# Kernel tuning notes

Measured on AMD Instinct MI355X. Metric: run time of the kernel, lower is better.

The kernel has to match this reference:

```python
import jax, jax.numpy as jnp
import numpy as np

EPS = 1e-5  # BatchNorm eps (torch default)

def setup_inputs() -> dict:
    key = jax.random.key(0)
    ks = jax.random.split(key, 12)
    B, C, H, W = 4, 256, 64, 64
    IC = 128  # inter_channels = C // 2
    s = 1.0 / np.sqrt(C)
    si = 1.0 / np.sqrt(IC)
    return {
        "x": jax.random.normal(ks[0], (B, C, H, W), jnp.float32),
        "y": jax.random.normal(ks[1], (B, C, H, W), jnp.float32),
        "g_w": jax.random.normal(ks[2], (IC, C), jnp.float32) * s,
        "g_b": jax.random.normal(ks[3], (IC,), jnp.float32) * 0.01,
        "dx_w": jax.random.normal(ks[4], (IC, C), jnp.float32) * s,
        "dx_b": jax.random.normal(ks[5], (IC,), jnp.float32) * 0.01,
        "dy_w": jax.random.normal(ks[6], (IC, C), jnp.float32) * s,
        "dy_b": jax.random.normal(ks[7], (IC,), jnp.float32) * 0.01,
        "w_w": jax.random.normal(ks[8], (C, IC), jnp.float32) * si,
        "w_b": jax.random.normal(ks[9], (C,), jnp.float32) * 0.01,
        "bn_gamma": jax.random.normal(ks[10], (C,), jnp.float32),
        "bn_beta": jax.random.normal(ks[11], (C,), jnp.float32) * 0.01,
    }

def _conv1x1(t, w, b):
    # t: [B,C,H,W], w: [O,C], b: [O] -> [B,O,H,W]
    return jnp.einsum('bchw,oc->bohw', t, w) + b[None, :, None, None]

def reference(x, y, g_w, g_b, dx_w, dx_b, dy_w, dy_b, w_w, w_b, bn_gamma, bn_beta):
    B, C, H, W = x.shape
    IC = g_w.shape[0]
    N = H * W
    g_y = _conv1x1(y, g_w, g_b).reshape(B, IC, N).transpose(0, 2, 1)      # [B,N,IC]
    theta_x = _conv1x1(x, dx_w, dx_b).reshape(B, IC, N).transpose(0, 2, 1)  # [B,N,IC]
    phi_y = _conv1x1(y, dy_w, dy_b).reshape(B, IC, N)                      # [B,IC,N]
    f = jnp.einsum('bnc,bcm->bnm', theta_x, phi_y)                         # [B,N,N]
    f_div_C = jax.nn.softmax(f, axis=-1)
    y2 = jnp.einsum('bnm,bmc->bnc', f_div_C, g_y)                          # [B,N,IC]
    y2 = y2.transpose(0, 2, 1).reshape(B, IC, H, W)
    wy = _conv1x1(y2, w_w, w_b)                                            # [B,C,H,W]
    # BatchNorm2d in training mode: batch stats over (B,H,W) per channel
    mean = jnp.mean(wy, axis=(0, 2, 3), keepdims=True)
    var = jnp.var(wy, axis=(0, 2, 3), keepdims=True)
    wy_bn = (wy - mean) / jnp.sqrt(var + EPS)
    wy_bn = wy_bn * bn_gamma[None, :, None, None] + bn_beta[None, :, None, None]
    return wy_bn + x
```

## Files before the change

kernel.cpp:

```cpp
#include <hip/hip_runtime.h>
#include <hip/hip_bf16.h>
#include <math.h>

typedef unsigned short ushort_t;
typedef __attribute__((ext_vector_type(8))) short     short8;
typedef __attribute__((ext_vector_type(8))) _Float16  half8;
typedef __attribute__((ext_vector_type(8))) unsigned short ushort8;
typedef __attribute__((ext_vector_type(4))) float     float4v;

__device__ __forceinline__ float b2f(ushort_t u) {
    return __uint_as_float(((unsigned)u) << 16);
}
__device__ __forceinline__ ushort_t f2b(float f) {
    unsigned i = __float_as_uint(f);
    return (ushort_t)((i + 0x7FFFu + ((i >> 16) & 1u)) >> 16);
}
__device__ __forceinline__ void split2(float v, ushort_t& h, ushort_t& l) {
    h = f2b(v);
    l = f2b(v - b2f(h));
}
__device__ __forceinline__ void glds16(const ushort_t* g, ushort_t* l) {
    __builtin_amdgcn_global_load_lds((const __attribute__((address_space(1))) void*)g,
                                     (__attribute__((address_space(3))) void*)l, 16, 0, 0);
}

#define WTFH_OFF   0
#define WTFL_OFF   196608
#define WWBH_OFF   393216
#define WWBL_OFF   458752
#define BIAS_OFF   524288
#define STATS_OFF  526336
#define PROJF_OFF  1048576
#define GT_OFF     9437184
#define OPART_OFF  13631488
#define WY_OFF     1048576

__global__ void prep_k(const float* __restrict__ dx_w, const float* __restrict__ dy_w,
                       const float* __restrict__ g_w,  const float* __restrict__ dx_b,
                       const float* __restrict__ dy_b, const float* __restrict__ g_b,
                       const float* __restrict__ w_w,
                       ushort_t* __restrict__ wtfh, ushort_t* __restrict__ wtfl,
                       ushort_t* __restrict__ wwbh, ushort_t* __restrict__ wwbl,
                       float* __restrict__ bias) {
    int idx = blockIdx.x * 256 + threadIdx.x;
    int j = idx & 7, lane = (idx >> 3) & 63, kk = (idx >> 9) & 7, ot = idx >> 12;
    int o = ot * 16 + (lane & 15);
    int c = kk * 32 + ((lane >> 4) * 8) + j;
    float v;
    if (o < 128)      v = dx_w[o * 256 + c];
    else if (o < 256) v = dy_w[(o - 128) * 256 + c];
    else              v = g_w[(o - 256) * 256 + c];
    ushort_t h, l;
    split2(v, h, l);
    wtfh[idx] = h; wtfl[idx] = l;
    if (idx < 32768) {
        split2(w_w[idx], h, l);
        wwbh[idx] = h; wwbl[idx] = l;
    }
    if (idx < 384) {
        bias[idx] = (idx < 128) ? dx_b[idx]
                  : (idx < 256) ? dy_b[idx - 128]
                                : g_b[idx - 256];
    }
}

__global__ __launch_bounds__(256) void proj_k(const float* __restrict__ x,
                                              const float* __restrict__ y,
                                              const ushort_t* __restrict__ wtfh,
                                              const ushort_t* __restrict__ wtfl,
                                              const float* __restrict__ bias,
                                              ushort_t* __restrict__ projf,
                                              ushort_t* __restrict__ gT) {
    __shared__ ushort_t xT[2][32 * 256];
    int b = blockIdx.y, n0 = blockIdx.x * 32;
    int tid = threadIdx.x;
    int w = tid >> 6, lane = tid & 63;
    int mrow = lane & 15, quad = lane >> 4, koff = quad * 8;
    int half = w & 1, sect = w >> 1;
    int arow = half * 16 + mrow;

    for (int s = 0; s < 2; s++) {
        if (s) __syncthreads();
        const float* src = s ? y : x;
        #pragma unroll
        for (int i = 0; i < 4; i++) {
            int ch = tid + i * 256;
            int c = ch >> 2, off = (ch & 3) * 8;
            const float* p = src + (size_t)(b * 256 + c) * 4096 + n0 + off;
            float4v v0 = *(const float4v*)p;
            float4v v1 = *(const float4v*)(p + 4);
            #pragma unroll
            for (int jj = 0; jj < 4; jj++) {
                ushort_t h, l;
                split2(v0[jj], h, l);
                xT[0][(off + jj) * 256 + c] = h;
                xT[1][(off + jj) * 256 + c] = l;
                split2(v1[jj], h, l);
                xT[0][(off + 4 + jj) * 256 + c] = h;
                xT[1][(off + 4 + jj) * 256 + c] = l;
            }
        }
        __syncthreads();

        short8 fh[8], fl[8];
        #pragma unroll
        for (int kk = 0; kk < 8; kk++) {
            fh[kk] = *(const short8*)&xT[0][arow * 256 + kk * 32 + koff];
            fl[kk] = *(const short8*)&xT[1][arow * 256 + kk * 32 + koff];
        }

        int ot0 = s ? (8 + sect * 8) : (sect * 4);
        int ot1 = s ? (ot0 + 8) : (ot0 + 4);
        for (int ot = ot0; ot < ot1; ot++) {
            float4v acc = {0.f, 0.f, 0.f, 0.f};
            #pragma unroll
            for (int kk = 0; kk < 8; kk++) {
                short8 bh = *(const short8*)(wtfh + (size_t)((ot * 8 + kk) * 64 + lane) * 8);
                short8 bl = *(const short8*)(wtfl + (size_t)((ot * 8 + kk) * 64 + lane) * 8);
                acc = __builtin_amdgcn_mfma_f32_16x16x32_bf16(fh[kk], bh, acc, 0, 0, 0);
                acc = __builtin_amdgcn_mfma_f32_16x16x32_bf16(fh[kk], bl, acc, 0, 0, 0);
                acc = __builtin_amdgcn_mfma_f32_16x16x32_bf16(fl[kk], bh, acc, 0, 0, 0);
            }
            int o = ot * 16 + mrow;
            float bo = bias[o];
            #pragma unroll
            for (int r = 0; r < 4; r++) {
                int n = n0 + half * 16 + quad * 4 + r;
                float v = acc[r] + bo;
                if (ot < 16) {
                    _Float16 hf = (_Float16)v;
                    projf[(size_t)(b * 4096 + n) * 256 + o] = *(ushort_t*)&hf;
                } else {
                    gT[(size_t)(b * 128 + (o - 256)) * 4096 + n] = f2b(v);
                }
            }
        }
    }
}

__global__ __launch_bounds__(512, 2) void flash_k(const ushort_t* __restrict__ projf,
                                                  const ushort_t* __restrict__ gT,
                                                  float* __restrict__ opart,
                                                  float* __restrict__ oml,
                                                  int kqlog) {
    __shared__ __align__(16) ushort_t KsF[2][8192];
    __shared__ __align__(16) ushort_t VsF[2][8192];
    __shared__ __align__(16) ushort_t Ps[256 * 72];

    int b = blockIdx.y;
    int kq = blockIdx.x & ((1 << kqlog) - 1);
    int q0 = (blockIdx.x >> kqlog) * 256;
    int iters = 64 >> kqlog;
    int kt0 = kq * iters;
    int tid = threadIdx.x, w = tid >> 6, lane = tid & 63;
    int mrow = lane & 15, quad = lane >> 4, koff = quad * 8;

    int kRow[2], kCol[2], vIc[2], vOf[2], dstB[2];
    #pragma unroll
    for (int i = 0; i < 2; i++) {
        int ck = tid + i * 512, combo = ck >> 6, l2 = ck & 63;
        kRow[i] = (combo >> 2) * 16 + (l2 & 15);
        kCol[i] = 128 + (combo & 3) * 32 + (l2 >> 4) * 8;
        vIc[i]  = (combo >> 1) * 16 + (l2 & 15);
        vOf[i]  = (combo & 1) * 32 + (l2 >> 4) * 8;
        dstB[i] = (i * 512 + w * 64) * 8;
    }

    half8 qf[2][4];
    #pragma unroll
    for (int s = 0; s < 2; s++)
        #pragma unroll
        for (int kk = 0; kk < 4; kk++)
            qf[s][kk] = *(const half8*)(projf + (size_t)(b * 4096 + q0 + w * 32 + s * 16 + mrow) * 256
                                        + kk * 32 + koff);

    float4v oacc[2][8], oaccL[2];
    #pragma unroll
    for (int s = 0; s < 2; s++) {
        oaccL[s] = (float4v){0.f, 0.f, 0.f, 0.f};
        #pragma unroll
        for (int ot = 0; ot < 8; ot++) oacc[s][ot] = (float4v){0.f, 0.f, 0.f, 0.f};
    }
    short8 vones;
    #pragma unroll
    for (int j = 0; j < 8; j++) vones[j] = (short)0x3F80;

    {
        int kb = kt0 * 64;
        #pragma unroll
        for (int i = 0; i < 2; i++) {
            glds16(projf + (size_t)(b * 4096 + kb + kRow[i]) * 256 + kCol[i], &KsF[0][dstB[i]]);
            glds16(gT + (size_t)(b * 128 + vIc[i]) * 4096 + kb + vOf[i], &VsF[0][dstB[i]]);
        }
    }

    for (int kt = kt0; kt < kt0 + iters; kt++) {
        int cur = (kt - kt0) & 1;
        __syncthreads();
        if (kt + 1 < kt0 + iters) {
            int kb = (kt + 1) * 64;
            #pragma unroll
            for (int i = 0; i < 2; i++) {
                glds16(projf + (size_t)(b * 4096 + kb + kRow[i]) * 256 + kCol[i], &KsF[1 - cur][dstB[i]]);
                glds16(gT + (size_t)(b * 128 + vIc[i]) * 4096 + kb + vOf[i], &VsF[1 - cur][dstB[i]]);
            }
        }

        float4v sacc[2][4];
        #pragma unroll
        for (int ct = 0; ct < 4; ct++) {
            float4v a0 = {0.f, 0.f, 0.f, 0.f}, a1 = {0.f, 0.f, 0.f, 0.f};
            #pragma unroll
            for (int kk = 0; kk < 4; kk++) {
                half8 bh = *(const half8*)&KsF[cur][((ct * 4 + kk) * 64 + lane) * 8];
                a0 = __builtin_amdgcn_mfma_f32_16x16x32_f16(qf[0][kk], bh, a0, 0, 0, 0);
                a1 = __builtin_amdgcn_mfma_f32_16x16x32_f16(qf[1][kk], bh, a1, 0, 0, 0);
            }
            sacc[0][ct] = a0; sacc[1][ct] = a1;
        }

        #pragma unroll
        for (int s = 0; s < 2; s++)
            #pragma unroll
            for (int r = 0; r < 4; r++) {
                int prow = w * 32 + s * 16 + quad * 4 + r;
                #pragma unroll
                for (int ct = 0; ct < 4; ct++) {
                    float p = __builtin_exp2f(fmaf(sacc[s][ct][r], 1.44269504f, -92.332481f));
                    Ps[prow * 72 + ct * 16 + mrow] = f2b(p);
                }
            }
        __builtin_amdgcn_s_waitcnt(0xC07F);

        #pragma unroll
        for (int k2 = 0; k2 < 2; k2++) {
            short8 a0 = *(const short8*)&Ps[(w * 32 + mrow) * 72 + k2 * 32 + koff];
            short8 a1 = *(const short8*)&Ps[(w * 32 + 16 + mrow) * 72 + k2 * 32 + koff];
            #pragma unroll
            for (int ot = 0; ot < 8; ot++) {
                short8 bfr = *(const short8*)&VsF[cur][((ot * 2 + k2) * 64 + lane) * 8];
                oacc[0][ot] = __builtin_amdgcn_mfma_f32_16x16x32_bf16(a0, bfr, oacc[0][ot], 0, 0, 0);
                oacc[1][ot] = __builtin_amdgcn_mfma_f32_16x16x32_bf16(a1, bfr, oacc[1][ot], 0, 0, 0);
            }
            oaccL[0] = __builtin_amdgcn_mfma_f32_16x16x32_bf16(a0, vones, oaccL[0], 0, 0, 0);
            oaccL[1] = __builtin_amdgcn_mfma_f32_16x16x32_bf16(a1, vones, oaccL[1], 0, 0, 0);
        }
    }

    #pragma unroll
    for (int s = 0; s < 2; s++)
        #pragma unroll
        for (int ot = 0; ot < 8; ot++)
            #pragma unroll
            for (int r = 0; r < 4; r++) {
                int R = b * 4096 + q0 + w * 32 + s * 16 + quad * 4 + r;
                opart[((size_t)kq * 16384 + R) * 128 + ot * 16 + mrow] = oacc[s][ot][r];
            }
    if (mrow == 0) {
        #pragma unroll
        for (int s = 0; s < 2; s++)
            #pragma unroll
            for (int r = 0; r < 4; r++) {
                int R = b * 4096 + q0 + w * 32 + s * 16 + quad * 4 + r;
                oml[kq * 16384 + R] = oaccL[s][r];
            }
    }
}

__global__ __launch_bounds__(256) void wy_k(const float* __restrict__ opart,
                                            const float* __restrict__ oml,
                                            const ushort_t* __restrict__ wwbh,
                                            const ushort_t* __restrict__ wwbl,
                                            const float* __restrict__ w_b,
                                            ushort_t* __restrict__ wy, int KQ) {
    int b = blockIdx.y, n0 = blockIdx.x * 32;
    int tid = threadIdx.x, w = tid >> 6, lane = tid & 63;
    int mrow = lane & 15, quad = lane >> 4, koff = quad * 8;
    int half = w & 1, sect = w >> 1;
    int Rn = b * 4096 + n0 + half * 16 + mrow;

    float L = 0.f;
    for (int kq = 0; kq < KQ; kq++) L += oml[kq * 16384 + Rn];
    float invL = 1.f / L;

    short8 bfh[4], bfl[4];
    #pragma unroll
    for (int kk = 0; kk < 4; kk++) {
        float a[8];
        #pragma unroll
        for (int j = 0; j < 8; j++) a[j] = 0.f;
        for (int kq = 0; kq < KQ; kq++) {
            const float* p = opart + ((size_t)kq * 16384 + Rn) * 128 + kk * 32 + koff;
            float4v v0 = *(const float4v*)p;
            float4v v1 = *(const float4v*)(p + 4);
            #pragma unroll
            for (int j = 0; j < 4; j++) { a[j] += v0[j]; a[4 + j] += v1[j]; }
        }
        #pragma unroll
        for (int j = 0; j < 8; j++) {
            ushort_t h, l;
            split2(a[j] * invL, h, l);
            bfh[kk][j] = (short)h; bfl[kk][j] = (short)l;
        }
    }

    int coln = n0 + half * 16 + mrow;
    for (int cot = sect * 8; cot < sect * 8 + 8; cot++) {
        float4v acc = {0.f, 0.f, 0.f, 0.f};
        #pragma unroll
        for (int kk = 0; kk < 4; kk++) {
            size_t woff = (size_t)(cot * 16 + mrow) * 128 + kk * 32 + koff;
            short8 ah = *(const short8*)(wwbh + woff);
            short8 al = *(const short8*)(wwbl + woff);
            acc = __builtin_amdgcn_mfma_f32_16x16x32_bf16(ah, bfh[kk], acc, 0, 0, 0);
            acc = __builtin_amdgcn_mfma_f32_16x16x32_bf16(ah, bfl[kk], acc, 0, 0, 0);
            acc = __builtin_amdgcn_mfma_f32_16x16x32_bf16(al, bfh[kk], acc, 0, 0, 0);
        }
        #pragma unroll
        for (int r = 0; r < 4; r++) {
            int co = cot * 16 + quad * 4 + r;
            wy[(size_t)(b * 256 + co) * 4096 + coln] = f2b(acc[r] + w_b[co]);
        }
    }
}

__global__ __launch_bounds__(256) void stats_k(const ushort_t* __restrict__ wy,
                                               float* __restrict__ stats) {
    __shared__ float red[8];
    int co = blockIdx.x, tid = threadIdx.x, w = tid >> 6, lane = tid & 63;
    float s = 0.f, s2 = 0.f;
    #pragma unroll
    for (int i = 0; i < 8; i++) {
        int ch = tid + i * 256;
        int b = ch >> 9, n = (ch & 511) * 8;
        ushort8 v = *(const ushort8*)(wy + (size_t)(b * 256 + co) * 4096 + n);
        #pragma unroll
        for (int j = 0; j < 8; j++) { float f = b2f(v[j]); s += f; s2 += f * f; }
    }
    #pragma unroll
    for (int d = 1; d < 64; d <<= 1) { s += __shfl_xor(s, d, 64); s2 += __shfl_xor(s2, d, 64); }
    if (lane == 0) { red[w] = s; red[4 + w] = s2; }
    __syncthreads();
    if (tid == 0) {
        stats[co]       = red[0] + red[1] + red[2] + red[3];
        stats[256 + co] = red[4] + red[5] + red[6] + red[7];
    }
}

__global__ __launch_bounds__(256) void bn_k(const ushort_t* __restrict__ wy,
                                            const float* __restrict__ x,
                                            const float* __restrict__ gamma,
                                            const float* __restrict__ beta,
                                            const float* __restrict__ stats,
                                            float* __restrict__ out) {
    int idx = (blockIdx.x * 256 + threadIdx.x) * 8;
    int c = (idx >> 12) & 255;
    const float inv_cnt = 1.f / 16384.f;
    float mean = stats[c] * inv_cnt;
    float var  = stats[256 + c] * inv_cnt - mean * mean;
    float inv  = rsqrtf(var + 1e-5f);
    float scale = gamma[c] * inv;
    float shift = beta[c] - mean * scale;
    ushort8 wv = *(const ushort8*)(wy + idx);
    float4v x0 = *(const float4v*)(x + idx);
    float4v x1 = *(const float4v*)(x + idx + 4);
    float4v o0, o1;
    #pragma unroll
    for (int j = 0; j < 4; j++) {
        o0[j] = b2f(wv[j]) * scale + shift + x0[j];
        o1[j] = b2f(wv[4 + j]) * scale + shift + x1[j];
    }
    *(float4v*)(out + idx) = o0;
    *(float4v*)(out + idx + 4) = o1;
}

extern "C" void kernel_launch(void* const* d_in, const int* in_sizes, int n_in,
                              void* d_out, int out_size, void* d_ws, size_t ws_size,
                              hipStream_t stream) {
    const float* x    = (const float*)d_in[0];
    const float* y    = (const float*)d_in[1];
    const float* g_w  = (const float*)d_in[2];
    const float* g_b  = (const float*)d_in[3];
    const float* dx_w = (const float*)d_in[4];
    const float* dx_b = (const float*)d_in[5];
    const float* dy_w = (const float*)d_in[6];
    const float* dy_b = (const float*)d_in[7];
    const float* w_w  = (const float*)d_in[8];
    const float* w_b  = (const float*)d_in[9];
    const float* bn_g = (const float*)d_in[10];
    const float* bn_b = (const float*)d_in[11];

    char* ws = (char*)d_ws;
    ushort_t* wtfh  = (ushort_t*)(ws + WTFH_OFF);
    ushort_t* wtfl  = (ushort_t*)(ws + WTFL_OFF);
    ushort_t* wwbh  = (ushort_t*)(ws + WWBH_OFF);
    ushort_t* wwbl  = (ushort_t*)(ws + WWBL_OFF);
    float*    bias  = (float*)(ws + BIAS_OFF);
    float*    stats = (float*)(ws + STATS_OFF);
    ushort_t* projf = (ushort_t*)(ws + PROJF_OFF);
    ushort_t* gT    = (ushort_t*)(ws + GT_OFF);
    float*    opart = (float*)(ws + OPART_OFF);
    ushort_t* wy    = (ushort_t*)(ws + WY_OFF);
    float*    out   = (float*)d_out;

    int kqlog;
    if      (ws_size >= 13631488u + 4u * (8388608u + 65536u)) kqlog = 2;
    else if (ws_size >= 13631488u + 2u * (8388608u + 65536u)) kqlog = 1;
    else                                                      kqlog = 0;
    int KQ = 1 << kqlog;
    float* oml = (float*)(ws + OPART_OFF + (size_t)KQ * 8388608u);

    prep_k<<<384, 256, 0, stream>>>(dx_w, dy_w, g_w, dx_b, dy_b, g_b, w_w,
                                    wtfh, wtfl, wwbh, wwbl, bias);
    proj_k<<<dim3(128, 4), 256, 0, stream>>>(x, y, wtfh, wtfl, bias, projf, gT);
    flash_k<<<dim3(16 << kqlog, 4), 512, 0, stream>>>(projf, gT, opart, oml, kqlog);
    wy_k<<<dim3(128, 4), 256, 0, stream>>>(opart, oml, wwbh, wwbl, w_b, wy, KQ);
    stats_k<<<256, 256, 0, stream>>>(wy, stats);
    bn_k<<<2048, 256, 0, stream>>>(wy, x, bn_g, bn_b, stats, out);
}
```

Measured before the change: 222.5 us.

## Split projection grid by output group and fuse BN stats into wy kernel

The projection kernel now gets a third grid dimension, so each block handles one of the theta, phi or g output groups. y is reloaded and re-split for the phi and g blocks, and the grid has three times as many blocks, which improves occupancy and parallelism. The separate BN statistics kernel is removed: wy_k reduces per-channel sum and sum of squares with shuffles and shared atomics, then adds them to global stats with atomics, and prep_k zeroes the stats. This saves a pass over wy and a kernel launch, at the cost of atomic contention and redundant input loads in proj_k.

```diff
diff --git a/kernel.cpp b/kernel.cpp
--- a/kernel.cpp
+++ b/kernel.cpp
@@ -41,7 +41,7 @@
                        const float* __restrict__ w_w,
                        ushort_t* __restrict__ wtfh, ushort_t* __restrict__ wtfl,
                        ushort_t* __restrict__ wwbh, ushort_t* __restrict__ wwbl,
-                       float* __restrict__ bias) {
+                       float* __restrict__ bias, float* __restrict__ stats) {
     int idx = blockIdx.x * 256 + threadIdx.x;
     int j = idx & 7, lane = (idx >> 3) & 63, kk = (idx >> 9) & 7, ot = idx >> 12;
     int o = ot * 16 + (lane & 15);
@@ -62,6 +62,7 @@
                   : (idx < 256) ? dy_b[idx - 128]
                                 : g_b[idx - 256];
     }
+    if (idx < 512) stats[idx] = 0.f;
 }
 
 __global__ __launch_bounds__(256) void proj_k(const float* __restrict__ x,
@@ -72,67 +73,63 @@
                                               ushort_t* __restrict__ projf,
                                               ushort_t* __restrict__ gT) {
     __shared__ ushort_t xT[2][32 * 256];
-    int b = blockIdx.y, n0 = blockIdx.x * 32;
+    int b = blockIdx.y, n0 = blockIdx.x * 32, z = blockIdx.z;
     int tid = threadIdx.x;
     int w = tid >> 6, lane = tid & 63;
     int mrow = lane & 15, quad = lane >> 4, koff = quad * 8;
     int half = w & 1, sect = w >> 1;
     int arow = half * 16 + mrow;
-
-    for (int s = 0; s < 2; s++) {
-        if (s) __syncthreads();
-        const float* src = s ? y : x;
-        #pragma unroll
-        for (int i = 0; i < 4; i++) {
-            int ch = tid + i * 256;
-            int c = ch >> 2, off = (ch & 3) * 8;
-            const float* p = src + (size_t)(b * 256 + c) * 4096 + n0 + off;
-            float4v v0 = *(const float4v*)p;
-            float4v v1 = *(const float4v*)(p + 4);
-            #pragma unroll
-            for (int jj = 0; jj < 4; jj++) {
-                ushort_t h, l;
-                split2(v0[jj], h, l);
-                xT[0][(off + jj) * 256 + c] = h;
-                xT[1][(off + jj) * 256 + c] = l;
-                split2(v1[jj], h, l);
-                xT[0][(off + 4 + jj) * 256 + c] = h;
-                xT[1][(off + 4 + jj) * 256 + c] = l;
-            }
-        }
-        __syncthreads();
-
-        short8 fh[8], fl[8];
+    const float* src = z ? y : x;
+
+    #pragma unroll
+    for (int i = 0; i < 4; i++) {
+        int ch = tid + i * 256;
+        int c = ch >> 2, off = (ch & 3) * 8;
+        const float* p = src + (size_t)(b * 256 + c) * 4096 + n0 + off;
+        float4v v0 = *(const float4v*)p;
+        float4v v1 = *(const float4v*)(p + 4);
+        #pragma unroll
+        for (int jj = 0; jj < 4; jj++) {
+            ushort_t h, l;
+            split2(v0[jj], h, l);
+            xT[0][(off + jj) * 256 + c] = h;
+            xT[1][(off + jj) * 256 + c] = l;
+            split2(v1[jj], h, l);
+            xT[0][(off + 4 + jj) * 256 + c] = h;
+            xT[1][(off + 4 + jj) * 256 + c] = l;
+        }
+    }
+    __syncthreads();
+
+    short8 fh[8], fl[8];
+    #pragma unroll
+    for (int kk = 0; kk < 8; kk++) {
+        fh[kk] = *(const short8*)&xT[0][arow * 256 + kk * 32 + koff];
+        fl[kk] = *(const short8*)&xT[1][arow * 256 + kk * 32 + koff];
+    }
+
+    int ot0 = z * 8 + sect * 4;
+    for (int ot = ot0; ot < ot0 + 4; ot++) {
+        float4v acc = {0.f, 0.f, 0.f, 0.f};
         #pragma unroll
         for (int kk = 0; kk < 8; kk++) {
-            fh[kk] = *(const short8*)&xT[0][arow * 256 + kk * 32 + koff];
-            fl[kk] = *(const short8*)&xT[1][arow * 256 + kk * 32 + koff];
-        }
-
-        int ot0 = s ? (8 + sect * 8) : (sect * 4);
-        int ot1 = s ? (ot0 + 8) : (ot0 + 4);
-        for (int ot = ot0; ot < ot1; ot++) {
-            float4v acc = {0.f, 0.f, 0.f, 0.f};
-            #pragma unroll
-            for (int kk = 0; kk < 8; kk++) {
-                short8 bh = *(const short8*)(wtfh + (size_t)((ot * 8 + kk) * 64 + lane) * 8);
-                short8 bl = *(const short8*)(wtfl + (size_t)((ot * 8 + kk) * 64 + lane) * 8);
-                acc = __builtin_amdgcn_mfma_f32_16x16x32_bf16(fh[kk], bh, acc, 0, 0, 0);
-                acc = __builtin_amdgcn_mfma_f32_16x16x32_bf16(fh[kk], bl, acc, 0, 0, 0);
-                acc = __builtin_amdgcn_mfma_f32_16x16x32_bf16(fl[kk], bh, acc, 0, 0, 0);
-            }
-            int o = ot * 16 + mrow;
-            float bo = bias[o];
-            #pragma unroll
-            for (int r = 0; r < 4; r++) {
-                int n = n0 + half * 16 + quad * 4 + r;
-                float v = acc[r] + bo;
-                if (ot < 16) {
-                    _Float16 hf = (_Float16)v;
-                    projf[(size_t)(b * 4096 + n) * 256 + o] = *(ushort_t*)&hf;
-                } else {
-                    gT[(size_t)(b * 128 + (o - 256)) * 4096 + n] = f2b(v);
-                }
+            short8 bh = *(const short8*)(wtfh + (size_t)((ot * 8 + kk) * 64 + lane) * 8);
+            short8 bl = *(const short8*)(wtfl + (size_t)((ot * 8 + kk) * 64 + lane) * 8);
+            acc = __builtin_amdgcn_mfma_f32_16x16x32_bf16(fh[kk], bh, acc, 0, 0, 0);
+            acc = __builtin_amdgcn_mfma_f32_16x16x32_bf16(fh[kk], bl, acc, 0, 0, 0);
+            acc = __builtin_amdgcn_mfma_f32_16x16x32_bf16(fl[kk], bh, acc, 0, 0, 0);
+        }
+        int o = ot * 16 + mrow;
+        float bo = bias[o];
+        #pragma unroll
+        for (int r = 0; r < 4; r++) {
+            int n = n0 + half * 16 + quad * 4 + r;
+            float v = acc[r] + bo;
+            if (z < 2) {
+                _Float16 hf = (_Float16)v;
+                projf[(size_t)(b * 4096 + n) * 256 + o] = *(ushort_t*)&hf;
+            } else {
+                gT[(size_t)(b * 128 + (o - 256)) * 4096 + n] = f2b(v);
             }
         }
     }
@@ -272,9 +269,13 @@
                                             const ushort_t* __restrict__ wwbh,
                                             const ushort_t* __restrict__ wwbl,
                                             const float* __restrict__ w_b,
-                                            ushort_t* __restrict__ wy, int KQ) {
+                                            ushort_t* __restrict__ wy,
+                                            float* __restrict__ stats, int KQ) {
+    __shared__ float s_sum[256], s_sq[256];
     int b = blockIdx.y, n0 = blockIdx.x * 32;
     int tid = threadIdx.x, w = tid >> 6, lane = tid & 63;
+    s_sum[tid] = 0.f; s_sq[tid] = 0.f;
+    __syncthreads();
     int mrow = lane & 15, quad = lane >> 4, koff = quad * 8;
     int half = w & 1, sect = w >> 1;
     int Rn = b * 4096 + n0 + half * 16 + mrow;
@@ -319,32 +320,20 @@
         #pragma unroll
         for (int r = 0; r < 4; r++) {
             int co = cot * 16 + quad * 4 + r;
-            wy[(size_t)(b * 256 + co) * 4096 + coln] = f2b(acc[r] + w_b[co]);
-        }
-    }
-}
-
-__global__ __launch_bounds__(256) void stats_k(const ushort_t* __restrict__ wy,
-                                               float* __restrict__ stats) {
-    __shared__ float red[8];
-    int co = blockIdx.x, tid = threadIdx.x, w = tid >> 6, lane = tid & 63;
-    float s = 0.f, s2 = 0.f;
-    #pragma unroll
-    for (int i = 0; i < 8; i++) {
-        int ch = tid + i * 256;
-        int b = ch >> 9, n = (ch & 511) * 8;
-        ushort8 v = *(const ushort8*)(wy + (size_t)(b * 256 + co) * 4096 + n);
-        #pragma unroll
-        for (int j = 0; j < 8; j++) { float f = b2f(v[j]); s += f; s2 += f * f; }
-    }
-    #pragma unroll
-    for (int d = 1; d < 64; d <<= 1) { s += __shfl_xor(s, d, 64); s2 += __shfl_xor(s2, d, 64); }
-    if (lane == 0) { red[w] = s; red[4 + w] = s2; }
+            float v = acc[r] + w_b[co];
+            wy[(size_t)(b * 256 + co) * 4096 + coln] = f2b(v);
+            float sv = v, sq = v * v;
+            #pragma unroll
+            for (int d = 1; d < 16; d <<= 1) {
+                sv += __shfl_xor(sv, d, 64);
+                sq += __shfl_xor(sq, d, 64);
+            }
+            if (mrow == 0) { atomicAdd(&s_sum[co], sv); atomicAdd(&s_sq[co], sq); }
+        }
+    }
     __syncthreads();
-    if (tid == 0) {
-        stats[co]       = red[0] + red[1] + red[2] + red[3];
-        stats[256 + co] = red[4] + red[5] + red[6] + red[7];
-    }
+    atomicAdd(&stats[tid], s_sum[tid]);
+    atomicAdd(&stats[256 + tid], s_sq[tid]);
 }
 
 __global__ __launch_bounds__(256) void bn_k(const ushort_t* __restrict__ wy,
@@ -411,10 +400,9 @@
     float* oml = (float*)(ws + OPART_OFF + (size_t)KQ * 8388608u);
 
     prep_k<<<384, 256, 0, stream>>>(dx_w, dy_w, g_w, dx_b, dy_b, g_b, w_w,
-                                    wtfh, wtfl, wwbh, wwbl, bias);
-    proj_k<<<dim3(128, 4), 256, 0, stream>>>(x, y, wtfh, wtfl, bias, projf, gT);
+                                    wtfh, wtfl, wwbh, wwbl, bias, stats);
+    proj_k<<<dim3(128, 4, 3), 256, 0, stream>>>(x, y, wtfh, wtfl, bias, projf, gT);
     flash_k<<<dim3(16 << kqlog, 4), 512, 0, stream>>>(projf, gT, opart, oml, kqlog);
-    wy_k<<<dim3(128, 4), 256, 0, stream>>>(opart, oml, wwbh, wwbl, w_b, wy, KQ);
-    stats_k<<<256, 256, 0, stream>>>(wy, stats);
+    wy_k<<<dim3(128, 4), 256, 0, stream>>>(opart, oml, wwbh, wwbl, w_b, wy, stats, KQ);
     bn_k<<<2048, 256, 0, stream>>>(wy, x, bn_g, bn_b, stats, out);
 }
```

Result: no change. 226.0 us (+1.6%).
